# Kernel optimization log

Hardware: AMD Instinct MI355X
Metric: run time of the kernel (lower is better)

## Reference

```python
import jax, jax.numpy as jnp
import numpy as np

B, T, DIM = 1, 1024, 1024
H = 8
QLR, KVLR = 768, 512
DNOPE, DROPE, DV = 128, 64, 128
DK = DNOPE + DROPE  # 192
EPS = 1e-5


def _rms(x, w):
    return x * jax.lax.rsqrt(jnp.mean(x * x, axis=-1, keepdims=True) + EPS) * w


def _l2norm(x):
    return x * jax.lax.rsqrt(jnp.sum(x * x, axis=-1, keepdims=True) + 1e-6)


def setup_inputs() -> dict:
    key = jax.random.key(0)
    ks = jax.random.split(key, 12)
    std = 0.02
    rnd = lambda k, shape: (jax.random.normal(k, shape, dtype=jnp.float32) * std)
    return {
        'x': jax.random.normal(ks[0], (B, T, DIM), dtype=jnp.float32),
        'cos': jax.random.normal(ks[1], (T, DROPE), dtype=jnp.float32),
        'sin': jax.random.normal(ks[2], (T, DROPE), dtype=jnp.float32),
        'wq_a': rnd(ks[3], (DIM, QLR)),
        'q_norm_w': jnp.ones((QLR,), dtype=jnp.float32),
        'wq_b': rnd(ks[4], (QLR, H * DK)),
        'wkv_a': rnd(ks[5], (DIM, KVLR + DROPE)),
        'kv_norm_w': jnp.ones((KVLR,), dtype=jnp.float32),
        'wkv_b': rnd(ks[6], (KVLR, H * (DNOPE + DV))),
        'wg_w': rnd(ks[7], (DIM, H * DK)),
        'wg_b': jnp.zeros((H * DK,), dtype=jnp.float32),
        'wb': rnd(ks[8], (DIM, H)),
        'wo': rnd(ks[9], (H * DV, DIM)),
    }


def _kda(q, k, v, g, beta):
    # q,k: [B,T,H,DK]; v: [B,T,H,DV]; g: [B,T,H,DK] (log-decay); beta: [B,T,H]
    q = _l2norm(q) * (DK ** -0.5)
    k = _l2norm(k)
    # time-major for scan
    qs = jnp.moveaxis(q, 1, 0)
    ks_ = jnp.moveaxis(k, 1, 0)
    vs = jnp.moveaxis(v, 1, 0)
    gs = jnp.moveaxis(g, 1, 0)
    bs = jnp.moveaxis(beta, 1, 0)

    def step(S, inp):
        q_t, k_t, v_t, g_t, b_t = inp  # [B,H,DK],[B,H,DK],[B,H,DV],[B,H,DK],[B,H]
        S = S * jnp.exp(g_t)[..., None]                       # per-key-dim decay
        u_t = b_t[..., None] * (v_t - jnp.einsum('bhk,bhkv->bhv', k_t, S))
        S = S + k_t[..., None] * u_t[..., None, :]            # rank-1 delta update
        o_t = jnp.einsum('bhk,bhkv->bhv', q_t, S)
        return S, o_t

    S0 = jnp.zeros((B, H, DK, DV), dtype=q.dtype)
    _, o = jax.lax.scan(step, S0, (qs, ks_, vs, gs, bs))
    return jnp.moveaxis(o, 0, 1)  # [B,T,H,DV]


def reference(x, cos, sin, wq_a, q_norm_w, wq_b, wkv_a, kv_norm_w, wkv_b, wg_w, wg_b, wb, wo):
    # cos/sin are accepted but unused, matching the original forward body.
    q = (_rms(x @ wq_a, q_norm_w) @ wq_b).reshape(B, T, H, DK)
    kv_all = x @ wkv_a
    kv_c, k_pe = kv_all[..., :KVLR], kv_all[..., KVLR:]       # [B,T,KVLR],[B,T,DROPE]
    kv = (_rms(kv_c, kv_norm_w) @ wkv_b).reshape(B, T, H, DNOPE + DV)
    k_nope, v = kv[..., :DNOPE], kv[..., DNOPE:]
    k = jnp.concatenate(
        [k_nope, jnp.broadcast_to(k_pe[:, :, None, :], (B, T, H, DROPE))], axis=-1)
    g = jax.nn.log_sigmoid(x @ wg_w + wg_b).reshape(B, T, H, DK)
    beta = jax.nn.sigmoid(x @ wb).reshape(B, T, H)
    o = _kda(q, k, v, g, beta)
    o = jnp.nan_to_num(o, nan=0.0, posinf=10000.0, neginf=-10000.0)
    return o.reshape(B, T, H * DV) @ wo
```

## Files before the change

kernel.cpp:

```cpp
#include <hip/hip_runtime.h>
#include <hip/hip_bf16.h>
#include <math.h>

#define TT 1024
#define DIM 1024
#define HH 8
#define QLR 768
#define KVLR 512
#define DNOPE 128
#define DROPE 64
#define DV 128
#define DK 192
#define HDK (HH*DK)
#define HKV (HH*(DNOPE+DV))
#define NBODY (TT/16)

#define OY   0
#define OQ   3072
#define OC   6144
#define OPL  9984
#define OU   10240
#define OLAM 12288
#define PABLK 12480

typedef __attribute__((ext_vector_type(8))) short short8;
typedef __attribute__((ext_vector_type(4))) float f32x4;

__device__ __forceinline__ unsigned short f2bf_rn(float f) {
    unsigned u = __float_as_uint(f);
    unsigned lsb = (u >> 16) & 1u;
    u += 0x7fffu + lsb;
    return (unsigned short)(u >> 16);
}
__device__ __forceinline__ float bf2f(unsigned short h) {
    return __uint_as_float(((unsigned)h) << 16);
}

__global__ __launch_bounds__(256) void wconv(
    const float* __restrict__ W0, unsigned short* __restrict__ H0,
    unsigned short* __restrict__ L0, int K0, int N0, int T0,
    const float* __restrict__ W1, unsigned short* __restrict__ H1,
    unsigned short* __restrict__ L1, int K1, int N1, int T1,
    const float* __restrict__ W2, unsigned short* __restrict__ H2,
    unsigned short* __restrict__ L2, int K2, int N2, int T2)
{
    __shared__ float Ls[64][65];
    int bx = blockIdx.x;
    const float* W; unsigned short* H; unsigned short* L; int K, N;
    if (bx < T0)           { W = W0; H = H0; L = L0; K = K0; N = N0; }
    else if (bx < T0 + T1) { bx -= T0; W = W1; H = H1; L = L1; K = K1; N = N1; }
    else                   { bx -= T0 + T1; W = W2; H = H2; L = L2; K = K2; N = N2; }

    const int NT = N >> 6;
    const int kt = bx / NT, nt = bx - kt * NT;
    const int k0 = kt * 64, n0 = nt * 64;
    const int tid = threadIdx.x;
    const int r = tid >> 2, c = (tid & 3) * 16;

#pragma unroll
    for (int i = 0; i < 4; i++)
        *(float4*)&Ls[r][c + i * 4] =
            *(const float4*)&W[(size_t)(k0 + r) * N + n0 + c + i * 4];
    __syncthreads();

    const int nr = tid >> 2, kc = (tid & 3) * 16;
    unsigned short hb[16], lb[16];
#pragma unroll
    for (int j = 0; j < 16; j++) {
        float v = Ls[kc + j][nr];
        unsigned short h = f2bf_rn(v);
        hb[j] = h;
        lb[j] = f2bf_rn(v - bf2f(h));
    }
    size_t ob = (size_t)(n0 + nr) * K + k0 + kc;
    *(float4*)&H[ob]     = ((float4*)hb)[0];
    *(float4*)&H[ob + 8] = ((float4*)hb)[1];
    *(float4*)&L[ob]     = ((float4*)lb)[0];
    *(float4*)&L[ob + 8] = ((float4*)lb)[1];
}

__global__ __launch_bounds__(256) void aconv(
    const float* __restrict__ A, unsigned short* __restrict__ H,
    unsigned short* __restrict__ L)
{
    int i = (blockIdx.x * 256 + threadIdx.x) * 8;
    float4 v0 = *(const float4*)&A[i];
    float4 v1 = *(const float4*)&A[i + 4];
    float vv[8] = {v0.x, v0.y, v0.z, v0.w, v1.x, v1.y, v1.z, v1.w};
    unsigned short hb[8], lb[8];
#pragma unroll
    for (int j = 0; j < 8; j++) {
        unsigned short h = f2bf_rn(vv[j]);
        hb[j] = h;
        lb[j] = f2bf_rn(vv[j] - bf2f(h));
    }
    *(float4*)&H[i] = *(float4*)hb;
    *(float4*)&L[i] = *(float4*)lb;
}

__global__ __launch_bounds__(128) void gemm_bt(
    const unsigned short* __restrict__ Ah0, const unsigned short* __restrict__ Al0,
    const unsigned short* __restrict__ Bh0, const unsigned short* __restrict__ Bl0,
    float* __restrict__ C0, int K0, int N0, int T0,
    const unsigned short* __restrict__ Ah1, const unsigned short* __restrict__ Al1,
    const unsigned short* __restrict__ Bh1, const unsigned short* __restrict__ Bl1,
    float* __restrict__ C1, int K1, int N1, int T1,
    const unsigned short* __restrict__ Ah2, const unsigned short* __restrict__ Al2,
    const unsigned short* __restrict__ Bh2, const unsigned short* __restrict__ Bl2,
    float* __restrict__ C2, int K2, int N2, int T2)
{
    __shared__ unsigned short Ahs[64 * 40], Als[64 * 40];
    __shared__ unsigned short Bhs[64 * 40], Bls[64 * 40];

    int bx = blockIdx.x;
    const unsigned short *Ah, *Al, *Bh, *Bl; float* C; int K, N;
    if (bx < T0) {
        Ah = Ah0; Al = Al0; Bh = Bh0; Bl = Bl0; C = C0; K = K0; N = N0;
    } else if (bx < T0 + T1) {
        bx -= T0; Ah = Ah1; Al = Al1; Bh = Bh1; Bl = Bl1; C = C1; K = K1; N = N1;
    } else {
        bx -= T0 + T1; Ah = Ah2; Al = Al2; Bh = Bh2; Bl = Bl2; C = C2; K = K2; N = N2;
    }

    const int tid = threadIdx.x;
    const int w = tid >> 6, l = tid & 63;
    const int q = l >> 4, m16 = l & 15;
    const int bm = blockIdx.y * 64, bn = bx * 64;

    const int c0i = tid * 2, c1i = tid * 2 + 1;
    const int r0 = c0i >> 2, o0 = (c0i & 3) * 8;
    const int r1 = c1i >> 2, o1 = (c1i & 3) * 8;
    const unsigned short* pAh0 = Ah + (size_t)(bm + r0) * K + o0;
    const unsigned short* pAh1 = Ah + (size_t)(bm + r1) * K + o1;
    const unsigned short* pAl0 = Al + (size_t)(bm + r0) * K + o0;
    const unsigned short* pAl1 = Al + (size_t)(bm + r1) * K + o1;
    const unsigned short* pBh0 = Bh + (size_t)(bn + r0) * K + o0;
    const unsigned short* pBh1 = Bh + (size_t)(bn + r1) * K + o1;
    const unsigned short* pBl0 = Bl + (size_t)(bn + r0) * K + o0;
    const unsigned short* pBl1 = Bl + (size_t)(bn + r1) * K + o1;

    f32x4 acc[2][4];
#pragma unroll
    for (int i = 0; i < 2; i++)
#pragma unroll
        for (int j = 0; j < 4; j++)
            acc[i][j] = (f32x4){0.f, 0.f, 0.f, 0.f};

    float4 vAh0 = *(const float4*)pAh0, vAh1 = *(const float4*)pAh1;
    float4 vAl0 = *(const float4*)pAl0, vAl1 = *(const float4*)pAl1;
    float4 vBh0 = *(const float4*)pBh0, vBh1 = *(const float4*)pBh1;
    float4 vBl0 = *(const float4*)pBl0, vBl1 = *(const float4*)pBl1;

    for (int k0 = 0;; k0 += 32) {
        __syncthreads();
        *(float4*)&Ahs[r0 * 40 + o0] = vAh0; *(float4*)&Ahs[r1 * 40 + o1] = vAh1;
        *(float4*)&Als[r0 * 40 + o0] = vAl0; *(float4*)&Als[r1 * 40 + o1] = vAl1;
        *(float4*)&Bhs[r0 * 40 + o0] = vBh0; *(float4*)&Bhs[r1 * 40 + o1] = vBh1;
        *(float4*)&Bls[r0 * 40 + o0] = vBl0; *(float4*)&Bls[r1 * 40 + o1] = vBl1;
        __syncthreads();

        const bool more = (k0 + 32) < K;
        if (more) {
            const int kn = k0 + 32;
            vAh0 = *(const float4*)(pAh0 + kn); vAh1 = *(const float4*)(pAh1 + kn);
            vAl0 = *(const float4*)(pAl0 + kn); vAl1 = *(const float4*)(pAl1 + kn);
            vBh0 = *(const float4*)(pBh0 + kn); vBh1 = *(const float4*)(pBh1 + kn);
            vBl0 = *(const float4*)(pBl0 + kn); vBl1 = *(const float4*)(pBl1 + kn);
        }

        short8 fah[2], fal[2], fbh[4], fbl[4];
#pragma unroll
        for (int mt = 0; mt < 2; mt++) {
            const int row = w * 32 + mt * 16 + m16;
            fah[mt] = *(const short8*)&Ahs[row * 40 + q * 8];
            fal[mt] = *(const short8*)&Als[row * 40 + q * 8];
        }
#pragma unroll
        for (int nt = 0; nt < 4; nt++) {
            const int row = nt * 16 + m16;
            fbh[nt] = *(const short8*)&Bhs[row * 40 + q * 8];
            fbl[nt] = *(const short8*)&Bls[row * 40 + q * 8];
        }
#pragma unroll
        for (int mt = 0; mt < 2; mt++)
#pragma unroll
            for (int nt = 0; nt < 4; nt++) {
                acc[mt][nt] = __builtin_amdgcn_mfma_f32_16x16x32_bf16(
                    fah[mt], fbh[nt], acc[mt][nt], 0, 0, 0);
                acc[mt][nt] = __builtin_amdgcn_mfma_f32_16x16x32_bf16(
                    fah[mt], fbl[nt], acc[mt][nt], 0, 0, 0);
                acc[mt][nt] = __builtin_amdgcn_mfma_f32_16x16x32_bf16(
                    fal[mt], fbh[nt], acc[mt][nt], 0, 0, 0);
            }
        if (!more) break;
    }

#pragma unroll
    for (int mt = 0; mt < 2; mt++)
#pragma unroll
        for (int nt = 0; nt < 4; nt++) {
            const int mrow = bm + w * 32 + mt * 16 + q * 4;
            const int ncol = bn + nt * 16 + m16;
#pragma unroll
            for (int r = 0; r < 4; r++)
                C[(size_t)(mrow + r) * N + ncol] = acc[mt][nt][r];
        }
}

__global__ __launch_bounds__(256) void rmsnorm_bf2(
    const float* __restrict__ in0, const float* __restrict__ w0,
    unsigned short* __restrict__ oh0, unsigned short* __restrict__ ol0,
    const float* __restrict__ in1, const float* __restrict__ w1,
    unsigned short* __restrict__ oh1, unsigned short* __restrict__ ol1)
{
    int bx = blockIdx.x;
    const float* in; const float* w; unsigned short *oh, *ol;
    int t, stride, ncols; float inv_n;
    if (bx < TT) {
        t = bx; in = in0; w = w0; oh = oh0; ol = ol0;
        stride = QLR; ncols = QLR; inv_n = 1.f / QLR;
    } else {
        t = bx - TT; in = in1; w = w1; oh = oh1; ol = ol1;
        stride = KVLR + DROPE; ncols = KVLR; inv_n = 1.f / KVLR;
    }
    const int tid = threadIdx.x;
    const float* row = in + (size_t)t * stride;
    float ss = 0.f;
    for (int c = tid; c < ncols; c += 256) { float v = row[c]; ss += v * v; }
#pragma unroll
    for (int m = 1; m < 64; m <<= 1) ss += __shfl_xor(ss, m);
    __shared__ float red[4];
    if ((tid & 63) == 0) red[tid >> 6] = ss;
    __syncthreads();
    float tot = red[0] + red[1] + red[2] + red[3];
    float scale = rsqrtf(tot * inv_n + 1e-5f);
    for (int c = tid; c < ncols; c += 256) {
        float v = row[c] * scale * w[c];
        unsigned short h = f2bf_rn(v);
        oh[(size_t)t * ncols + c] = h;
        ol[(size_t)t * ncols + c] = f2bf_rn(v - bf2f(h));
    }
}

__global__ __launch_bounds__(256) void small_fused(
    const float* __restrict__ g, const float* __restrict__ bias,
    float* __restrict__ la_h,
    const float* __restrict__ x, const float* __restrict__ wb,
    float* __restrict__ betab,
    const float* __restrict__ qraw, const float* __restrict__ kvb,
    const float* __restrict__ kv_all, float* __restrict__ q_h,
    float* __restrict__ k_h)
{
    int bx = blockIdx.x;
    if (bx < 6144) {
        int i = bx * 256 + threadIdx.x;
        int t = i / HDK, col = i - t * HDK;
        int h = col / DK, d = col - h * DK;
        float z = g[i] + bias[col];
        float la = fminf(z, 0.f) - log1pf(__expf(-fabsf(z)));
        la_h[((size_t)h * TT + t) * DK + d] = la;
        return;
    }
    bx -= 6144;
    const int lane = threadIdx.x & 63, wv = threadIdx.x >> 6;
    if (bx < 2048) {
        const int p = bx * 4 + wv;
        const int t = p >> 3, h = p & 7;
        const float* xr = x + (size_t)t * DIM;
        float s = 0.f;
        for (int e = lane; e < DIM; e += 64) s += xr[e] * wb[e * HH + h];
#pragma unroll
        for (int m = 1; m < 64; m <<= 1) s += __shfl_xor(s, m);
        if (lane == 0) betab[p] = 1.f / (1.f + expf(-s));
        return;
    }
    bx -= 2048;
    {
        const int p = bx * 4 + wv;
        const int t = p >> 3, h = p & 7;

        const float* qrow = qraw + (size_t)t * HDK + h * DK;
        float q0 = qrow[lane], q1 = qrow[lane + 64], q2 = qrow[lane + 128];
        float ss = q0 * q0 + q1 * q1 + q2 * q2;
#pragma unroll
        for (int m = 1; m < 64; m <<= 1) ss += __shfl_xor(ss, m);
        float sc = rsqrtf(ss + 1e-6f) * 0.07216878364870323f;
        float* qo = q_h + ((size_t)h * TT + t) * DK;
        qo[lane] = q0 * sc; qo[lane + 64] = q1 * sc; qo[lane + 128] = q2 * sc;

        const float* knope = kvb + (size_t)t * HKV + h * (DNOPE + DV);
        float k0 = knope[lane], k1 = knope[lane + 64];
        float k2 = kv_all[(size_t)t * (KVLR + DROPE) + KVLR + lane];
        float ks = k0 * k0 + k1 * k1 + k2 * k2;
#pragma unroll
        for (int m = 1; m < 64; m <<= 1) ks += __shfl_xor(ks, m);
        float kc = rsqrtf(ks + 1e-6f);
        float* ko = k_h + ((size_t)h * TT + t) * DK;
        ko[lane] = k0 * kc; ko[lane + 64] = k1 * kc; ko[lane + 128] = k2 * kc;
    }
}

__device__ __forceinline__ float dpp_xor1(float x) {
    return __int_as_float(__builtin_amdgcn_update_dpp(
        0, __float_as_int(x), 0xB1, 0xF, 0xF, false));
}
__device__ __forceinline__ float dpp_xor2(float x) {
    return __int_as_float(__builtin_amdgcn_update_dpp(
        0, __float_as_int(x), 0x4E, 0xF, 0xF, false));
}
__device__ __forceinline__ float dpp_hm(float x) {
    return __int_as_float(__builtin_amdgcn_update_dpp(
        0, __float_as_int(x), 0x141, 0xF, 0xF, false));
}
__device__ __forceinline__ float dpp_rm(float x) {
    return __int_as_float(__builtin_amdgcn_update_dpp(
        0, __float_as_int(x), 0x140, 0xF, 0xF, false));
}
__device__ __forceinline__ float dpp_b15(float x) {
    return __int_as_float(__builtin_amdgcn_update_dpp(
        0, __float_as_int(x), 0x142, 0xF, 0xF, false));
}
__device__ __forceinline__ float red32v(float x) {
    x += dpp_xor1(x);
    x += dpp_xor2(x);
    x += dpp_hm(x);
    x += dpp_rm(x);
    x += dpp_b15(x);
    return x;
}

__device__ __forceinline__ void gl_lds16(const float* g, float* l) {
    __builtin_amdgcn_global_load_lds(
        (const __attribute__((address_space(1))) void*)g,
        (__attribute__((address_space(3))) void*)l, 16, 0, 0);
}

__global__ __launch_bounds__(256) void chunk_prep(
    const float* __restrict__ k_h, const float* __restrict__ la_h,
    const float* __restrict__ q_h, const float* __restrict__ kvb,
    const float* __restrict__ betab, float* __restrict__ pa)
{
    __shared__ float Ls[16][196];
    __shared__ float Ks[16][196];
    __shared__ float Qs[16][196];
    __shared__ float Ws[16][196];
    __shared__ float Xs[16][196];
    __shared__ float Ms[16][16];
    __shared__ float bs[16];

    const int tid = threadIdx.x;
    const int n = blockIdx.x >> 3, h = blockIdx.x & 7;
    const size_t g0 = ((size_t)h * TT + n * 16) * DK;
    float* blob = pa + (size_t)blockIdx.x * PABLK;

#pragma unroll
    for (int s = 0; s < 3; s++) {
        int off = (tid * 3 + s) * 4;
        int r = off / 192, c = off - r * 192;
        *(float4*)&Ks[r][c] = *(const float4*)(k_h + g0 + off);
        *(float4*)&Ls[r][c] = *(const float4*)(la_h + g0 + off);
        *(float4*)&Qs[r][c] = *(const float4*)(q_h + g0 + off);
    }
    if (tid < 16) bs[tid] = betab[(size_t)(n * 16 + tid) * HH + h];
    __syncthreads();

    if (tid < 192) {
        float g = 0.f;
#pragma unroll
        for (int i = 0; i < 16; i++) { g += Ls[i][tid]; Ls[i][tid] = g; }
    }
    __syncthreads();

#pragma unroll
    for (int s = 0; s < 12; s++) {
        int idx = s * 256 + tid;
        int i = idx / 192, d = idx - i * 192;
        float G = Ls[i][d];
        float eg = __expf(G), en = __expf(-G);
        float kk = Ks[i][d];
        Ws[i][d] = bs[i] * kk * eg;
        Qs[i][d] *= eg;
        Ks[i][d] = kk * en;
    }
    __syncthreads();

#pragma unroll
    for (int s = 0; s < 3; s++) {
        int off = (tid * 3 + s) * 4;
        int r = off / 192, c = off - r * 192;
        *(float4*)(blob + OQ + off) = *(const float4*)&Qs[r][c];
    }
    if (tid < 192) {
        float lam = __expf(Ls[15][tid]);
        blob[OLAM + tid] = lam;
#pragma unroll
        for (int j4 = 0; j4 < 4; j4++) {
            float4 v;
            v.x = Ks[j4 * 4 + 0][tid] * lam; v.y = Ks[j4 * 4 + 1][tid] * lam;
            v.z = Ks[j4 * 4 + 2][tid] * lam; v.w = Ks[j4 * 4 + 3][tid] * lam;
            *(float4*)(blob + OC + tid * 20 + j4 * 4) = v;
        }
        blob[OC + tid * 20 + 16] = lam;
        blob[OC + tid * 20 + 17] = 0.f;
        blob[OC + tid * 20 + 18] = 0.f; blob[OC + tid * 20 + 19] = 0.f;
    }
    {
        const int i = tid >> 4, j = tid & 15;
        float m = 0.f, p = 0.f;
#pragma unroll
        for (int d4 = 0; d4 < 48; d4++) {
            float4 w  = *(const float4*)&Ws[i][d4 * 4];
            float4 ka = *(const float4*)&Ks[j][d4 * 4];
            float4 qa = *(const float4*)&Qs[i][d4 * 4];
            m += w.x * ka.x + w.y * ka.y + w.z * ka.z + w.w * ka.w;
            p += qa.x * ka.x + qa.y * ka.y + qa.z * ka.z + qa.w * ka.w;
        }
        Ms[i][j] = (j < i) ? m : 0.f;
        blob[OPL + tid] = (j <= i) ? p : 0.f;
    }
    __syncthreads();

    float y[16], uu[16];
    const bool doY = (tid < 192);
    const bool doU = (tid >= 128);
    const int dcol = tid, ccol = tid - 128;
    if (doY) {
#pragma unroll
        for (int i = 0; i < 16; i++) y[i] = Ws[i][dcol];
#pragma unroll
        for (int i = 1; i < 16; i++)
#pragma unroll
            for (int j = 0; j < i; j++)
                y[i] = fmaf(-Ms[i][j], y[j], y[i]);
    }
    if (doU) {
#pragma unroll
        for (int i = 0; i < 16; i++)
            uu[i] = bs[i] * kvb[(size_t)(n * 16 + i) * HKV + h * (DNOPE + DV) + DNOPE + ccol];
#pragma unroll
        for (int i = 1; i < 16; i++)
#pragma unroll
            for (int j = 0; j < i; j++)
                uu[i] = fmaf(-Ms[i][j], uu[j], uu[i]);
    }
    if (doY) {
#pragma unroll
        for (int i = 0; i < 16; i++) Xs[i][dcol] = y[i];
    }
    __syncthreads();
#pragma unroll
    for (int s = 0; s < 3; s++) {
        int off = (tid * 3 + s) * 4;
        int r = off / 192, c = off - r * 192;
        *(float4*)(blob + OY + off) = *(const float4*)&Xs[r][c];
    }
    if (doU) {
#pragma unroll
        for (int i4 = 0; i4 < 4; i4++) {
            float4 t;
            t.x = uu[i4 * 4 + 0]; t.y = uu[i4 * 4 + 1];
            t.z = uu[i4 * 4 + 2]; t.w = uu[i4 * 4 + 3];
            *(float4*)(blob + OU + (size_t)ccol * 16 + i4 * 4) = t;
        }
    }
}

__global__ __launch_bounds__(1024) void kda_chunk(
    const float* __restrict__ pa, unsigned short* __restrict__ obh,
    unsigned short* __restrict__ obl)
{
    __shared__ float Cb[3][3840];
    __shared__ float Pb[3][256];
    __shared__ float ubs[3][64];
    __shared__ float lbs[3][192];
    __shared__ float Ss[784];
    __shared__ float us[80];

    const int tid = threadIdx.x;
    const int w = tid >> 6, lane = tid & 63;
    const int h = blockIdx.x & 7, cg = blockIdx.x >> 3;
    const int c0 = cg * 4;

    const int ti  = w;
    const int ccs = lane >> 5;
    const int dg  = lane & 31;
    const int dbase = dg * 6;

    auto stage = [&](int buf, int n) {
        const float* blob = pa + (size_t)(n * 8 + h) * PABLK;
        if (w < 15) {
            gl_lds16(blob + OC + w * 256 + lane * 4, &Cb[buf][w * 256]);
        } else {
            gl_lds16(blob + OPL + lane * 4, &Pb[buf][0]);
            if (lane < 16)
                gl_lds16(blob + OU + c0 * 16 + lane * 4, &ubs[buf][0]);
            if (lane < 48)
                gl_lds16(blob + OLAM + lane * 4, &lbs[buf][0]);
        }
    };

    auto ldYQ = [&](int n, float2 (&Y)[3], float2 (&Q)[3]) {
        const float* blob = pa + (size_t)(n * 8 + h) * PABLK;
        const float* py_ = blob + OY + ti * 192 + dbase;
        const float* pq_ = blob + OQ + ti * 192 + dbase;
#pragma unroll
        for (int s = 0; s < 3; s++) {
            Y[s] = *(const float2*)(py_ + s * 2);
            Q[s] = *(const float2*)(pq_ + s * 2);
        }
    };

    auto P1 = [&](int sbase, int bf, float2 (&Yr)[3], float2 (&Qr)[3]) -> float {
        const int r = sbase + ccs;
        const float* Sp = &Ss[r * 196 + dbase];
        float2 s0 = *(const float2*)Sp;
        float2 s1 = *(const float2*)(Sp + 2);
        float2 s2 = *(const float2*)(Sp + 4);
        float ubv = ubs[bf][r * 16 + ti];
        float py0 = Yr[0].x * s0.x, py1 = Yr[0].y * s0.y;
        float pq0 = Qr[0].x * s0.x, pq1 = Qr[0].y * s0.y;
        py0 = fmaf(Yr[1].x, s1.x, py0); py1 = fmaf(Yr[1].y, s1.y, py1);
        pq0 = fmaf(Qr[1].x, s1.x, pq0); pq1 = fmaf(Qr[1].y, s1.y, pq1);
        py0 = fmaf(Yr[2].x, s2.x, py0); py1 = fmaf(Yr[2].y, s2.y, py1);
        pq0 = fmaf(Qr[2].x, s2.x, pq0); pq1 = fmaf(Qr[2].y, s2.y, pq1);
        float zy = red32v(py0 + py1);
        float zq = red32v(pq0 + pq1);
        if (dg == 31) us[r * 20 + ti] = ubv - zy;
        return zq;
    };

    auto P2 = [&](int sbase, int bf, int n, float zq) {
        const int r = sbase + ccs;
        float pbvv = Pb[bf][ti * 16 + (dg & 15)];
        float usv  = us[r * 20 + (dg & 15)];
        float acc = (dg <= ti) ? pbvv * usv : 0.f;
        acc = red32v(acc);
        if (dg == 31) {
            float ov = zq + acc;
            if (isnan(ov)) ov = 0.f;
            else if (isinf(ov)) ov = ov > 0.f ? 1e4f : -1e4f;
            size_t oi = (size_t)(n * 16 + ti) * (HH * DV) + h * DV + c0 + r;
            unsigned short hb = f2bf_rn(ov);
            obh[oi] = hb;
            obl[oi] = f2bf_rn(ov - bf2f(hb));
        }
        if (tid < 384) {
            const int d = tid >> 1, c = (tid & 1) + sbase;
            const float4* up4 = (const float4*)&us[c * 20];
            float4 u0 = up4[0], u1 = up4[1], u2v = up4[2], u3 = up4[3];
            float svv = Ss[c * 196 + d];
            const float4* C4 = (const float4*)&Cb[bf][d * 20];
            float4 k0 = C4[0], k1 = C4[1], k2 = C4[2], k3 = C4[3];
            float a0 = lbs[bf][d] * svv, a1 = 0.f;
            a0 = fmaf(k0.x, u0.x,  a0); a1 = fmaf(k0.y, u0.y,  a1);
            a0 = fmaf(k0.z, u0.z,  a0); a1 = fmaf(k0.w, u0.w,  a1);
            a0 = fmaf(k1.x, u1.x,  a0); a1 = fmaf(k1.y, u1.y,  a1);
            a0 = fmaf(k1.z, u1.z,  a0); a1 = fmaf(k1.w, u1.w,  a1);
            a0 = fmaf(k2.x, u2v.x, a0); a1 = fmaf(k2.y, u2v.y, a1);
            a0 = fmaf(k2.z, u2v.z, a0); a1 = fmaf(k2.w, u2v.w, a1);
            a0 = fmaf(k3.x, u3.x,  a0); a1 = fmaf(k3.y, u3.y,  a1);
            a0 = fmaf(k3.z, u3.z,  a0); a1 = fmaf(k3.w, u3.w,  a1);
            Ss[c * 196 + d] = a0 + a1;
        }
    };

#define SEG_BAR asm volatile("s_waitcnt lgkmcnt(0)\n\ts_barrier" ::: "memory")

    float zqA, zqB;
    float2 Ya[3], Qa[3], Yb[3], Qb[3];

    for (int idx = tid; idx < 784; idx += 1024) Ss[idx] = 0.f;
    stage(0, 0);
    stage(1, 1);
    asm volatile("" ::: "memory");
    ldYQ(0, Ya, Qa);
    asm volatile("s_waitcnt vmcnt(0) lgkmcnt(0)\n\ts_barrier" ::: "memory");
    zqA = P1(0, 0, Ya, Qa);
    SEG_BAR;

    int bf = 0;
    for (int n = 0; n < 62; n += 2) {
        int bf1 = bf + 1; if (bf1 >= 3) bf1 -= 3;
        int bf2 = bf + 2; if (bf2 >= 3) bf2 -= 3;
        stage(bf2, n + 2);
        asm volatile("" ::: "memory");
        ldYQ(n + 1, Yb, Qb);
        zqB = P1(2, bf, Ya, Qa);
        P2(0, bf, n, zqA);
        SEG_BAR;
        zqA = P1(0, bf1, Yb, Qb);
        P2(2, bf, n, zqB);
        SEG_BAR;
        stage(bf, n + 3);
        asm volatile("" ::: "memory");
        ldYQ(n + 2, Ya, Qa);
        zqB = P1(2, bf1, Yb, Qb);
        P2(0, bf1, n + 1, zqA);
        SEG_BAR;
        zqA = P1(0, bf2, Ya, Qa);
        P2(2, bf1, n + 1, zqB);
        SEG_BAR;
        bf = bf2;
    }
    {
        int bf1 = bf + 1; if (bf1 >= 3) bf1 -= 3;
        ldYQ(63, Yb, Qb);
        zqB = P1(2, bf, Ya, Qa);
        P2(0, bf, 62, zqA);
        SEG_BAR;
        zqA = P1(0, bf1, Yb, Qb);
        P2(2, bf, 62, zqB);
        SEG_BAR;
        zqB = P1(2, bf1, Yb, Qb);
        P2(0, bf1, 63, zqA);
        SEG_BAR;
        P2(2, bf1, 63, zqB);
    }
#undef SEG_BAR
}

extern "C" void kernel_launch(void* const* d_in, const int* in_sizes, int n_in,
                              void* d_out, int out_size, void* d_ws, size_t ws_size,
                              hipStream_t stream)
{
    const float* x         = (const float*)d_in[0];
    const float* wq_a      = (const float*)d_in[3];
    const float* q_norm_w  = (const float*)d_in[4];
    const float* wq_b      = (const float*)d_in[5];
    const float* wkv_a     = (const float*)d_in[6];
    const float* kv_norm_w = (const float*)d_in[7];
    const float* wkv_b     = (const float*)d_in[8];
    const float* wg_w      = (const float*)d_in[9];
    const float* wg_b      = (const float*)d_in[10];
    const float* wb        = (const float*)d_in[11];
    const float* wo        = (const float*)d_in[12];
    float* out = (float*)d_out;

    float* ws = (float*)d_ws;
    float* xq     = ws;
    float* kv_all = xq     + TT * QLR;
    float* agraw  = kv_all + TT * (KVLR + DROPE);
    float* qnraw  = agraw  + TT * HDK;
    float* kvb    = qnraw  + TT * HDK;
    float* la_h   = kvb    + TT * HKV;
    float* q_h    = la_h   + TT * HDK;
    float* k_h    = q_h    + TT * HDK;
    float* betab  = k_h    + TT * HDK;
    float* pa     = betab  + TT * HH;
    float* tail   = pa     + 512 * PABLK;

    unsigned short* wo_h  = (unsigned short*)tail;
    unsigned short* wo_l  = wo_h  + 1048576;
    unsigned short* xh    = wo_l  + 1048576;
    unsigned short* xl    = xh    + 1048576;
    unsigned short* xqh   = xl    + 1048576;
    unsigned short* xql   = xqh   + 786432;
    unsigned short* kvnh  = xql   + 786432;
    unsigned short* kvnl  = kvnh  + 524288;

    unsigned short* wqa_h  = (unsigned short*)pa;
    unsigned short* wqa_l  = wqa_h  + 786432;
    unsigned short* wkva_h = wqa_l  + 786432;
    unsigned short* wkva_l = wkva_h + 589824;
    unsigned short* wgw_h  = wkva_l + 589824;
    unsigned short* wgw_l  = wgw_h  + 1572864;
    unsigned short* wqb_h  = wgw_l  + 1572864;
    unsigned short* wqb_l  = wqb_h  + 1179648;
    unsigned short* wkvb_h = wqb_l  + 1179648;
    unsigned short* wkvb_l = wkvb_h + 1048576;

    unsigned short* obh = (unsigned short*)agraw;
    unsigned short* obl = obh + 1048576;

    dim3 blk(256);

    wconv<<<dim3(192 + 144 + 384), blk, 0, stream>>>(
        wq_a, wqa_h, wqa_l, DIM, QLR, 192,
        wkv_a, wkva_h, wkva_l, DIM, KVLR + DROPE, 144,
        wg_w, wgw_h, wgw_l, DIM, HDK, 384);
    wconv<<<dim3(288 + 256 + 256), blk, 0, stream>>>(
        wq_b, wqb_h, wqb_l, QLR, HDK, 288,
        wkv_b, wkvb_h, wkvb_l, KVLR, HKV, 256,
        wo, wo_h, wo_l, DIM, DIM, 256);

    aconv<<<dim3(TT * DIM / (256 * 8)), blk, 0, stream>>>(x, xh, xl);

    gemm_bt<<<dim3(12 + 9 + 24, 16), dim3(128), 0, stream>>>(
        xh, xl, wqa_h, wqa_l, xq, DIM, QLR, 12,
        xh, xl, wkva_h, wkva_l, kv_all, DIM, KVLR + DROPE, 9,
        xh, xl, wgw_h, wgw_l, agraw, DIM, HDK, 24);

    rmsnorm_bf2<<<dim3(2 * TT), blk, 0, stream>>>(
        xq, q_norm_w, xqh, xql,
        kv_all, kv_norm_w, kvnh, kvnl);

    gemm_bt<<<dim3(24 + 32, 16), dim3(128), 0, stream>>>(
        xqh, xql, wqb_h, wqb_l, qnraw, QLR, HDK, 24,
        kvnh, kvnl, wkvb_h, wkvb_l, kvb, KVLR, HKV, 32,
        xh, xl, wqa_h, wqa_l, xq, DIM, QLR, 0);

    small_fused<<<dim3(6144 + 2048 + 2048), blk, 0, stream>>>(
        agraw, wg_b, la_h,
        x, wb, betab,
        qnraw, kvb, kv_all, q_h, k_h);

    chunk_prep<<<512, blk, 0, stream>>>(k_h, la_h, q_h, kvb, betab, pa);
    kda_chunk<<<256, dim3(1024), 0, stream>>>(pa, obh, obl);

    gemm_bt<<<dim3(16, 16), dim3(128), 0, stream>>>(
        obh, obl, wo_h, wo_l, out, DIM, DIM, 16,
        xh, xl, wqa_h, wqa_l, xq, DIM, QLR, 0,
        xh, xl, wqa_h, wqa_l, xq, DIM, QLR, 0);
}
```

Before: 313.3 us.

## Fuse gate log-sigmoid, beta, and q/k L2-norm into chunk_prep

Removes the small_fused kernel and moves its work into chunk_prep. Each chunk block now computes log-sigmoid of the gate, the beta projection from x and wb, and the q/k L2 normalisation directly from the raw GEMM outputs. This drops one launch and the write and re-read of the la_h, q_h, k_h and betab intermediates. In exchange chunk_prep does more work per block, including a serial 1024-length dot product per row for beta. The obh buffer is moved to a spare region because agraw is now read by chunk_prep.

```diff
diff --git a/kernel.cpp b/kernel.cpp
--- a/kernel.cpp
+++ b/kernel.cpp
@@ -13,7 +13,6 @@
 #define DK 192
 #define HDK (HH*DK)
 #define HKV (HH*(DNOPE+DV))
-#define NBODY (TT/16)
 
 #define OY   0
 #define OQ   3072
@@ -242,64 +241,6 @@
     }
 }
 
-__global__ __launch_bounds__(256) void small_fused(
-    const float* __restrict__ g, const float* __restrict__ bias,
-    float* __restrict__ la_h,
-    const float* __restrict__ x, const float* __restrict__ wb,
-    float* __restrict__ betab,
-    const float* __restrict__ qraw, const float* __restrict__ kvb,
-    const float* __restrict__ kv_all, float* __restrict__ q_h,
-    float* __restrict__ k_h)
-{
-    int bx = blockIdx.x;
-    if (bx < 6144) {
-        int i = bx * 256 + threadIdx.x;
-        int t = i / HDK, col = i - t * HDK;
-        int h = col / DK, d = col - h * DK;
-        float z = g[i] + bias[col];
-        float la = fminf(z, 0.f) - log1pf(__expf(-fabsf(z)));
-        la_h[((size_t)h * TT + t) * DK + d] = la;
-        return;
-    }
-    bx -= 6144;
-    const int lane = threadIdx.x & 63, wv = threadIdx.x >> 6;
-    if (bx < 2048) {
-        const int p = bx * 4 + wv;
-        const int t = p >> 3, h = p & 7;
-        const float* xr = x + (size_t)t * DIM;
-        float s = 0.f;
-        for (int e = lane; e < DIM; e += 64) s += xr[e] * wb[e * HH + h];
-#pragma unroll
-        for (int m = 1; m < 64; m <<= 1) s += __shfl_xor(s, m);
-        if (lane == 0) betab[p] = 1.f / (1.f + expf(-s));
-        return;
-    }
-    bx -= 2048;
-    {
-        const int p = bx * 4 + wv;
-        const int t = p >> 3, h = p & 7;
-
-        const float* qrow = qraw + (size_t)t * HDK + h * DK;
-        float q0 = qrow[lane], q1 = qrow[lane + 64], q2 = qrow[lane + 128];
-        float ss = q0 * q0 + q1 * q1 + q2 * q2;
-#pragma unroll
-        for (int m = 1; m < 64; m <<= 1) ss += __shfl_xor(ss, m);
-        float sc = rsqrtf(ss + 1e-6f) * 0.07216878364870323f;
-        float* qo = q_h + ((size_t)h * TT + t) * DK;
-        qo[lane] = q0 * sc; qo[lane + 64] = q1 * sc; qo[lane + 128] = q2 * sc;
-
-        const float* knope = kvb + (size_t)t * HKV + h * (DNOPE + DV);
-        float k0 = knope[lane], k1 = knope[lane + 64];
-        float k2 = kv_all[(size_t)t * (KVLR + DROPE) + KVLR + lane];
-        float ks = k0 * k0 + k1 * k1 + k2 * k2;
-#pragma unroll
-        for (int m = 1; m < 64; m <<= 1) ks += __shfl_xor(ks, m);
-        float kc = rsqrtf(ks + 1e-6f);
-        float* ko = k_h + ((size_t)h * TT + t) * DK;
-        ko[lane] = k0 * kc; ko[lane + 64] = k1 * kc; ko[lane + 128] = k2 * kc;
-    }
-}
-
 __device__ __forceinline__ float dpp_xor1(float x) {
     return __int_as_float(__builtin_amdgcn_update_dpp(
         0, __float_as_int(x), 0xB1, 0xF, 0xF, false));
@@ -319,6 +260,13 @@
 __device__ __forceinline__ float dpp_b15(float x) {
     return __int_as_float(__builtin_amdgcn_update_dpp(
         0, __float_as_int(x), 0x142, 0xF, 0xF, false));
+}
+__device__ __forceinline__ float red16(float x) {
+    x += dpp_xor1(x);
+    x += dpp_xor2(x);
+    x += dpp_hm(x);
+    x += dpp_rm(x);
+    return x;
 }
 __device__ __forceinline__ float red32v(float x) {
     x += dpp_xor1(x);
@@ -336,9 +284,10 @@
 }
 
 __global__ __launch_bounds__(256) void chunk_prep(
-    const float* __restrict__ k_h, const float* __restrict__ la_h,
-    const float* __restrict__ q_h, const float* __restrict__ kvb,
-    const float* __restrict__ betab, float* __restrict__ pa)
+    const float* __restrict__ qnraw, const float* __restrict__ agraw,
+    const float* __restrict__ wg_b, const float* __restrict__ kvb,
+    const float* __restrict__ kv_all, const float* __restrict__ x,
+    const float* __restrict__ wb, float* __restrict__ pa)
 {
     __shared__ float Ls[16][196];
     __shared__ float Ks[16][196];
@@ -347,23 +296,69 @@
     __shared__ float Xs[16][196];
     __shared__ float Ms[16][16];
     __shared__ float bs[16];
+    __shared__ float kn[16], qn[16];
 
     const int tid = threadIdx.x;
     const int n = blockIdx.x >> 3, h = blockIdx.x & 7;
-    const size_t g0 = ((size_t)h * TT + n * 16) * DK;
+    const int t0 = n * 16;
     float* blob = pa + (size_t)blockIdx.x * PABLK;
 
 #pragma unroll
     for (int s = 0; s < 3; s++) {
         int off = (tid * 3 + s) * 4;
         int r = off / 192, c = off - r * 192;
-        *(float4*)&Ks[r][c] = *(const float4*)(k_h + g0 + off);
-        *(float4*)&Ls[r][c] = *(const float4*)(la_h + g0 + off);
-        *(float4*)&Qs[r][c] = *(const float4*)(q_h + g0 + off);
-    }
-    if (tid < 16) bs[tid] = betab[(size_t)(n * 16 + tid) * HH + h];
+        *(float4*)&Qs[r][c] =
+            *(const float4*)(qnraw + (size_t)(t0 + r) * HDK + h * DK + c);
+        float4 g4 = *(const float4*)(agraw + (size_t)(t0 + r) * HDK + h * DK + c);
+        float4 b4 = *(const float4*)(wg_b + h * DK + c);
+        float4 la;
+        {
+            float z;
+            z = g4.x + b4.x; la.x = fminf(z, 0.f) - log1pf(__expf(-fabsf(z)));
+            z = g4.y + b4.y; la.y = fminf(z, 0.f) - log1pf(__expf(-fabsf(z)));
+            z = g4.z + b4.z; la.z = fminf(z, 0.f) - log1pf(__expf(-fabsf(z)));
+            z = g4.w + b4.w; la.w = fminf(z, 0.f) - log1pf(__expf(-fabsf(z)));
+        }
+        *(float4*)&Ls[r][c] = la;
+        float4 kv;
+        if (c < DNOPE)
+            kv = *(const float4*)(kvb + (size_t)(t0 + r) * HKV + h * (DNOPE + DV) + c);
+        else
+            kv = *(const float4*)(kv_all + (size_t)(t0 + r) * (KVLR + DROPE) + KVLR + (c - DNOPE));
+        *(float4*)&Ks[r][c] = kv;
+    }
+    {
+        const int lane = tid & 63, wv = tid >> 6;
+#pragma unroll
+        for (int rr = 0; rr < 4; rr++) {
+            const int r = wv * 4 + rr;
+            const float* xr = x + (size_t)(t0 + r) * DIM;
+            float ssum = 0.f;
+            for (int e = lane; e < DIM; e += 64) ssum += xr[e] * wb[e * HH + h];
+#pragma unroll
+            for (int m = 1; m < 64; m <<= 1) ssum += __shfl_xor(ssum, m);
+            if (lane == 0) bs[r] = 1.f / (1.f + expf(-ssum));
+        }
+    }
     __syncthreads();
 
+    {
+        const int i = tid >> 4, j = tid & 15;
+        float sq = 0.f, sk = 0.f;
+#pragma unroll
+        for (int c4 = 0; c4 < 3; c4++) {
+            float4 q4 = *(const float4*)&Qs[i][j * 12 + c4 * 4];
+            float4 k4 = *(const float4*)&Ks[i][j * 12 + c4 * 4];
+            sq += q4.x * q4.x + q4.y * q4.y + q4.z * q4.z + q4.w * q4.w;
+            sk += k4.x * k4.x + k4.y * k4.y + k4.z * k4.z + k4.w * k4.w;
+        }
+        sq = red16(sq);
+        sk = red16(sk);
+        if (j == 0) {
+            qn[i] = rsqrtf(sq + 1e-6f) * 0.07216878364870323f;
+            kn[i] = rsqrtf(sk + 1e-6f);
+        }
+    }
     if (tid < 192) {
         float g = 0.f;
 #pragma unroll
@@ -377,9 +372,9 @@
         int i = idx / 192, d = idx - i * 192;
         float G = Ls[i][d];
         float eg = __expf(G), en = __expf(-G);
-        float kk = Ks[i][d];
+        float kk = Ks[i][d] * kn[i];
         Ws[i][d] = bs[i] * kk * eg;
-        Qs[i][d] *= eg;
+        Qs[i][d] = Qs[i][d] * qn[i] * eg;
         Ks[i][d] = kk * en;
     }
     __syncthreads();
@@ -436,7 +431,7 @@
     if (doU) {
 #pragma unroll
         for (int i = 0; i < 16; i++)
-            uu[i] = bs[i] * kvb[(size_t)(n * 16 + i) * HKV + h * (DNOPE + DV) + DNOPE + ccol];
+            uu[i] = bs[i] * kvb[(size_t)(t0 + i) * HKV + h * (DNOPE + DV) + DNOPE + ccol];
 #pragma unroll
         for (int i = 1; i < 16; i++)
 #pragma unroll
@@ -642,11 +637,8 @@
     float* agraw  = kv_all + TT * (KVLR + DROPE);
     float* qnraw  = agraw  + TT * HDK;
     float* kvb    = qnraw  + TT * HDK;
-    float* la_h   = kvb    + TT * HKV;
-    float* q_h    = la_h   + TT * HDK;
-    float* k_h    = q_h    + TT * HDK;
-    float* betab  = k_h    + TT * HDK;
-    float* pa     = betab  + TT * HH;
+    float* spare  = kvb    + TT * HKV;
+    float* pa     = spare  + 3 * TT * HDK + TT * HH;
     float* tail   = pa     + 512 * PABLK;
 
     unsigned short* wo_h  = (unsigned short*)tail;
@@ -669,7 +661,7 @@
     unsigned short* wkvb_h = wqb_l  + 1179648;
     unsigned short* wkvb_l = wkvb_h + 1048576;
 
-    unsigned short* obh = (unsigned short*)agraw;
+    unsigned short* obh = (unsigned short*)spare;
     unsigned short* obl = obh + 1048576;
 
     dim3 blk(256);
@@ -699,12 +691,8 @@
         kvnh, kvnl, wkvb_h, wkvb_l, kvb, KVLR, HKV, 32,
         xh, xl, wqa_h, wqa_l, xq, DIM, QLR, 0);
 
-    small_fused<<<dim3(6144 + 2048 + 2048), blk, 0, stream>>>(
-        agraw, wg_b, la_h,
-        x, wb, betab,
-        qnraw, kvb, kv_all, q_h, k_h);
-
-    chunk_prep<<<512, blk, 0, stream>>>(k_h, la_h, q_h, kvb, betab, pa);
+    chunk_prep<<<512, blk, 0, stream>>>(
+        qnraw, agraw, wg_b, kvb, kv_all, x, wb, pa);
     kda_chunk<<<256, dim3(1024), 0, stream>>>(pa, obh, obl);
 
     gemm_bt<<<dim3(16, 16), dim3(128), 0, stream>>>(
```

New measurement: 313.0 us. Within noise of the previous version (-0.1%).
